# Performance work log

Measured on AMD Instinct MI355X. Metric: run time of the kernel, lower is better.

## Reference

```python
import jax, jax.numpy as jnp
import numpy as np

EPS = 1e-5
QB = 127.0  # int8 activation quantization bound

def rmsnorm(x):
    # SimpleRMSNorm: x / rms(x), no learned scale
    return x * jax.lax.rsqrt(jnp.mean(x * x, axis=-1, keepdims=True) + EPS)

def activation_quant(x):
    # per-token absmax int8 quant-dequant
    scale = QB / jnp.clip(jnp.max(jnp.abs(x), axis=-1, keepdims=True), EPS)
    return jnp.clip(jnp.round(x * scale), -QB - 1, QB) / scale

def weight_quant(w):
    # per-tensor ternary quant-dequant (BitNet b1.58)
    scale = 1.0 / jnp.clip(jnp.mean(jnp.abs(w)), EPS)
    return jnp.clip(jnp.round(w * scale), -1.0, 1.0) / scale

def ste(x, q):
    # straight-through estimator: forward uses q, gradient flows to x
    return x + jax.lax.stop_gradient(q - x)

def bitlinear(x, w, b):
    xn = rmsnorm(x)
    xq = ste(xn, activation_quant(xn))
    wq = ste(w, weight_quant(w))
    # x: [b, s, d_in], w: [d_out, d_in] -> [b, s, d_out]
    return jnp.einsum('bsd,od->bso', xq, wq) + b

def setup_inputs() -> dict:
    key = jax.random.key(0)
    k1, k2, k3, k4, k5 = jax.random.split(key, 5)
    dim, inner = 1024, 4096
    x = jax.random.normal(k1, (4, 4096, dim), dtype=jnp.float32)
    w1 = jax.random.normal(k2, (inner, dim), dtype=jnp.float32) * (dim ** -0.5)
    b1 = jax.random.normal(k3, (inner,), dtype=jnp.float32) * 0.02
    w2 = jax.random.normal(k4, (dim, inner), dtype=jnp.float32) * (inner ** -0.5)
    b2 = jax.random.normal(k5, (dim,), dtype=jnp.float32) * 0.02
    return {"x": x, "w1": w1, "b1": b1, "w2": w2, "b2": b2}

def reference(x, w1, b1, w2, b2):
    h = jax.nn.gelu(bitlinear(x, w1, b1), approximate=False)  # torch nn.GELU default = exact erf
    # dropout p=0.0 is identity; post_act_ln disabled
    return bitlinear(h, w2, b2)
```

## Files before the change

### kernel.cpp

```cpp
#include <hip/hip_runtime.h>
#include <hip/hip_bf16.h>

#define TOK   16384
#define DIM   1024
#define INNER 4096
#define EPSF  1e-5f

typedef int v4i  __attribute__((ext_vector_type(4)));
typedef int v16i __attribute__((ext_vector_type(16)));

static __device__ __forceinline__ void async_copy16(const char* g, char* l) {
    __builtin_amdgcn_global_load_lds(
        (const __attribute__((address_space(1))) unsigned int*)g,
        (__attribute__((address_space(3))) unsigned int*)l, 16, 0, 0);
}

static __device__ __forceinline__ float bf2f(unsigned short u) {
    return __uint_as_float(((unsigned)u) << 16);
}
static __device__ __forceinline__ unsigned short f2bf(float f) {
    unsigned u = __float_as_uint(f);
    return (unsigned short)((u + 0x7fffu + ((u >> 16) & 1u)) >> 16);
}

static __device__ __forceinline__ float fast_erf(float z) {
    float az = fabsf(z);
    float tt = __builtin_amdgcn_rcpf(1.f + 0.3275911f * az);
    float poly = ((((1.061405429f * tt - 1.453152027f) * tt + 1.421413741f) * tt
                   - 0.284496736f) * tt + 0.254829592f) * tt;
    float er = 1.f - poly * __expf(-az * az);
    return copysignf(er, z);
}

static __device__ __forceinline__ float waveSum(float v) {
#pragma unroll
    for (int o = 32; o > 0; o >>= 1) v += __shfl_down(v, o, 64);
    return v;
}
static __device__ __forceinline__ float waveMax(float v) {
#pragma unroll
    for (int o = 32; o > 0; o >>= 1) v = fmaxf(v, __shfl_down(v, o, 64));
    return v;
}

__global__ void absmean_k(const float* __restrict__ w, int n4, float* __restrict__ acc) {
    int idx = blockIdx.x * blockDim.x + threadIdx.x;
    int stride = gridDim.x * blockDim.x;
    const float4* w4 = (const float4*)w;
    float s = 0.f;
    for (int i = idx; i < n4; i += stride) {
        float4 v = w4[i];
        s += fabsf(v.x) + fabsf(v.y) + fabsf(v.z) + fabsf(v.w);
    }
    __shared__ float sp[4];
    int wv = threadIdx.x >> 6, lane = threadIdx.x & 63;
    s = waveSum(s);
    if (lane == 0) sp[wv] = s;
    __syncthreads();
    if (threadIdx.x == 0) atomicAdd(acc, sp[0] + sp[1] + sp[2] + sp[3]);
}

__global__ void wquant_k(const float* __restrict__ w, int n,
                         const float* __restrict__ acc, float* __restrict__ wscale,
                         char* __restrict__ wq) {
    float mean = *acc / (float)n;
    float cl = fmaxf(mean, EPSF);
    float s = 1.f / cl;
    if (blockIdx.x == 0 && threadIdx.x == 0) *wscale = cl;
    int idx = blockIdx.x * blockDim.x + threadIdx.x;
    int stride = gridDim.x * blockDim.x;
    int n4 = n >> 2;
    const float4* w4 = (const float4*)w;
    unsigned* q4 = (unsigned*)wq;
    for (int i = idx; i < n4; i += stride) {
        float4 v = w4[i];
        float e[4] = {v.x, v.y, v.z, v.w};
        unsigned packed = 0;
#pragma unroll
        for (int j = 0; j < 4; j++) {
            float r = rintf(e[j] * s);
            r = fminf(fmaxf(r, -1.f), 1.f);
            packed |= ((unsigned)((int)r & 0xff)) << (8 * j);
        }
        q4[i] = packed;
    }
}

template <int D, int VPT>
__global__ void actquant_f32_k(const float* __restrict__ X, char* __restrict__ Q,
                               float* __restrict__ rs_out) {
    int token = blockIdx.x;
    int t = threadIdx.x;
    const float4* xp = (const float4*)(X + (long)token * D);
    float vals[VPT];
    float ss = 0.f, am = 0.f;
#pragma unroll
    for (int j = 0; j < VPT / 4; j++) {
        float4 v = xp[t * (VPT / 4) + j];
        vals[4 * j] = v.x; vals[4 * j + 1] = v.y; vals[4 * j + 2] = v.z; vals[4 * j + 3] = v.w;
        ss += v.x * v.x + v.y * v.y + v.z * v.z + v.w * v.w;
        am = fmaxf(am, fmaxf(fmaxf(fabsf(v.x), fabsf(v.y)), fmaxf(fabsf(v.z), fabsf(v.w))));
    }
    __shared__ float sp[8];
    __shared__ float bc[2];
    int wv = t >> 6, lane = t & 63;
    float S = waveSum(ss);
    float M = waveMax(am);
    if (lane == 0) { sp[wv] = S; sp[4 + wv] = M; }
    __syncthreads();
    if (t == 0) {
        float Sa = sp[0] + sp[1] + sp[2] + sp[3];
        float Ma = fmaxf(fmaxf(sp[4], sp[5]), fmaxf(sp[6], sp[7]));
        float rinv = rsqrtf(Sa * (1.f / (float)D) + EPSF);
        float amn = Ma * rinv;
        float scale = 127.f / fmaxf(amn, EPSF);
        rs_out[token] = 1.f / scale;
        bc[0] = rinv; bc[1] = scale;
    }
    __syncthreads();
    float rinv = bc[0], scale = bc[1];
    unsigned outw[VPT / 4];
#pragma unroll
    for (int j = 0; j < VPT; j++) {
        float r = rintf((vals[j] * rinv) * scale);
        r = fminf(fmaxf(r, -128.f), 127.f);
        unsigned qi = (unsigned)((int)r & 0xff) << (8 * (j & 3));
        if ((j & 3) == 0) outw[j / 4] = qi; else outw[j / 4] |= qi;
    }
    unsigned* qp = (unsigned*)(Q + (long)token * D);
#pragma unroll
    for (int j = 0; j < VPT / 4; j++) qp[t * (VPT / 4) + j] = outw[j];
}

template <int D, int VPT>
__global__ void actquant_bf16_k(const unsigned short* __restrict__ X, char* __restrict__ Q,
                                float* __restrict__ rs_out) {
    int token = blockIdx.x;
    int t = threadIdx.x;
    const uint4* xp = (const uint4*)(X + (long)token * D);
    float vals[VPT];
    float ss = 0.f, am = 0.f;
#pragma unroll
    for (int j = 0; j < VPT / 8; j++) {
        uint4 v = xp[t * (VPT / 8) + j];
        unsigned ws[4] = {v.x, v.y, v.z, v.w};
#pragma unroll
        for (int p = 0; p < 4; p++) {
            float f0 = bf2f((unsigned short)(ws[p] & 0xffff));
            float f1 = bf2f((unsigned short)(ws[p] >> 16));
            vals[8 * j + 2 * p] = f0; vals[8 * j + 2 * p + 1] = f1;
            ss += f0 * f0 + f1 * f1;
            am = fmaxf(am, fmaxf(fabsf(f0), fabsf(f1)));
        }
    }
    __shared__ float sp[8];
    __shared__ float bc[2];
    int wv = t >> 6, lane = t & 63;
    float S = waveSum(ss);
    float M = waveMax(am);
    if (lane == 0) { sp[wv] = S; sp[4 + wv] = M; }
    __syncthreads();
    if (t == 0) {
        float Sa = sp[0] + sp[1] + sp[2] + sp[3];
        float Ma = fmaxf(fmaxf(sp[4], sp[5]), fmaxf(sp[6], sp[7]));
        float rinv = rsqrtf(Sa * (1.f / (float)D) + EPSF);
        float amn = Ma * rinv;
        float scale = 127.f / fmaxf(amn, EPSF);
        rs_out[token] = 1.f / scale;
        bc[0] = rinv; bc[1] = scale;
    }
    __syncthreads();
    float rinv = bc[0], scale = bc[1];
    unsigned outw[4];
#pragma unroll
    for (int j = 0; j < VPT; j++) {
        float r = rintf((vals[j] * rinv) * scale);
        r = fminf(fmaxf(r, -128.f), 127.f);
        unsigned qi = (unsigned)((int)r & 0xff) << (8 * (j & 3));
        if ((j & 3) == 0) outw[j / 4] = qi; else outw[j / 4] |= qi;
    }
    uint4* qp = (uint4*)(Q + (long)token * D);
    qp[t] = make_uint4(outw[0], outw[1], outw[2], outw[3]);
}

template <int DO_GELU, int OUT_F32>
__global__ __launch_bounds__(256, 2) void gemm_i8_k(
    const char* __restrict__ A, const char* __restrict__ Bw,
    const float* __restrict__ rs, const float* __restrict__ wscale_p,
    const float* __restrict__ bias, void* __restrict__ outp,
    int M, int N, int K) {
    __shared__ char As[2][16384];
    __shared__ char Bs[2][8192];
    int t = threadIdx.x;
    int n0 = blockIdx.x * 128, m0 = blockIdx.y * 256;
    int wv = t >> 6, lane = t & 63;
    int l31 = lane & 31, kh = lane >> 5;
    int wm = (wv & 1) * 128, wn = (wv >> 1) * 64;

    int r = t >> 2;
    const char* aps[4];
    const char* bps[2];
#pragma unroll
    for (int c = 0; c < 4; c++) {
        int row = c * 64 + r;
        int src = (t & 3) ^ ((row >> 1) & 3);
        aps[c] = A + (long)(m0 + row) * K + src * 16;
    }
#pragma unroll
    for (int c = 0; c < 2; c++) {
        int row = c * 64 + r;
        int src = (t & 3) ^ ((row >> 1) & 3);
        bps[c] = Bw + (long)(n0 + row) * K + src * 16;
    }

    v16i acc[4][2] = {};
    int aidx[4][2], bidx[2][2];
#pragma unroll
    for (int i = 0; i < 4; i++) {
        int row = wm + i * 32 + l31;
        int sw = (row >> 1) & 3;
#pragma unroll
        for (int ks = 0; ks < 2; ks++) aidx[i][ks] = row * 4 + ((ks * 2 + kh) ^ sw);
    }
#pragma unroll
    for (int j = 0; j < 2; j++) {
        int row = wn + j * 32 + l31;
        int sw = (row >> 1) & 3;
#pragma unroll
        for (int ks = 0; ks < 2; ks++) bidx[j][ks] = row * 4 + ((ks * 2 + kh) ^ sw);
    }

    auto issue = [&](int it, int buf) {
        long k0 = (long)it << 6;
#pragma unroll
        for (int c = 0; c < 4; c++) async_copy16(aps[c] + k0, As[buf] + c * 4096 + t * 16);
#pragma unroll
        for (int c = 0; c < 2; c++) async_copy16(bps[c] + k0, Bs[buf] + c * 4096 + t * 16);
    };

    int nIt = K >> 6;
    issue(0, 0);
    for (int it = 0; it < nIt; ++it) {
        int cur = it & 1;
        if (it + 1 < nIt) {
            issue(it + 1, cur ^ 1);
            asm volatile("s_waitcnt vmcnt(6)" ::: "memory");
        } else {
            asm volatile("s_waitcnt vmcnt(0)" ::: "memory");
        }
        asm volatile("s_barrier" ::: "memory");
        const v4i* As4 = (const v4i*)As[cur];
        const v4i* Bs4 = (const v4i*)Bs[cur];
#pragma unroll
        for (int ks = 0; ks < 2; ks++) {
            v4i a[4], b[2];
#pragma unroll
            for (int i = 0; i < 4; i++) a[i] = As4[aidx[i][ks]];
#pragma unroll
            for (int j = 0; j < 2; j++) b[j] = Bs4[bidx[j][ks]];
#pragma unroll
            for (int i = 0; i < 4; i++)
#pragma unroll
                for (int j = 0; j < 2; j++)
                    acc[i][j] = __builtin_amdgcn_mfma_i32_32x32x32_i8(a[i], b[j], acc[i][j], 0, 0, 0);
        }
        asm volatile("s_barrier" ::: "memory");
    }

    float wsc = *wscale_p;
    float bv[2];
#pragma unroll
    for (int j = 0; j < 2; j++) bv[j] = bias[n0 + wn + j * 32 + l31];
#pragma unroll
    for (int i = 0; i < 4; i++) {
        int mbase = m0 + wm + i * 32 + 4 * kh;
        float fsv[16];
#pragma unroll
        for (int rg = 0; rg < 16; rg++)
            fsv[rg] = rs[mbase + (rg & 3) + 8 * (rg >> 2)] * wsc;
#pragma unroll
        for (int j = 0; j < 2; j++) {
            int ng = n0 + wn + j * 32 + l31;
#pragma unroll
            for (int rg = 0; rg < 16; rg++) {
                int mg = mbase + (rg & 3) + 8 * (rg >> 2);
                float v = (float)acc[i][j][rg] * fsv[rg] + bv[j];
                if (DO_GELU) v = 0.5f * v * (1.f + fast_erf(v * 0.70710678118654752f));
                long idx = (long)mg * N + ng;
                if (OUT_F32) ((float*)outp)[idx] = v;
                else ((unsigned short*)outp)[idx] = f2bf(v);
            }
        }
    }
}

extern "C" void kernel_launch(void* const* d_in, const int* in_sizes, int n_in,
                              void* d_out, int out_size, void* d_ws, size_t ws_size,
                              hipStream_t stream) {
    const float* x  = (const float*)d_in[0];
    const float* w1 = (const float*)d_in[1];
    const float* b1 = (const float*)d_in[2];
    const float* w2 = (const float*)d_in[3];
    const float* b2 = (const float*)d_in[4];
    float* out = (float*)d_out;

    char* ws = (char*)d_ws;
    float* acc1 = (float*)(ws + 0);
    float* acc2 = (float*)(ws + 4);
    float* wsc1 = (float*)(ws + 8);
    float* wsc2 = (float*)(ws + 12);
    size_t off = 256;
    char* w1q = ws + off; off += (size_t)INNER * DIM;
    char* w2q = ws + off; off += (size_t)INNER * DIM;
    char* xq1 = ws + off; off += (size_t)TOK * DIM;
    float* rs1 = (float*)(ws + off); off += (size_t)TOK * 4;
    char* xq2 = ws + off; off += (size_t)TOK * INNER;
    float* rs2 = (float*)(ws + off); off += (size_t)TOK * 4;
    unsigned short* h = (unsigned short*)(ws + off);

    hipMemsetAsync(d_ws, 0, 16, stream);

    int nw = INNER * DIM;
    absmean_k<<<1024, 256, 0, stream>>>(w1, nw / 4, acc1);
    absmean_k<<<1024, 256, 0, stream>>>(w2, nw / 4, acc2);
    wquant_k<<<2048, 256, 0, stream>>>(w1, nw, acc1, wsc1, w1q);
    wquant_k<<<2048, 256, 0, stream>>>(w2, nw, acc2, wsc2, w2q);

    actquant_f32_k<DIM, 4><<<TOK, 256, 0, stream>>>(x, xq1, rs1);
    gemm_i8_k<1, 0><<<dim3(INNER / 128, TOK / 256), 256, 0, stream>>>(
        xq1, w1q, rs1, wsc1, b1, (void*)h, TOK, INNER, DIM);
    actquant_bf16_k<INNER, 16><<<TOK, 256, 0, stream>>>(h, xq2, rs2);
    gemm_i8_k<0, 1><<<dim3(DIM / 128, TOK / 256), 256, 0, stream>>>(
        xq2, w2q, rs2, wsc2, b2, (void*)out, TOK, DIM, INNER);
}
```

Measured before the change: 421.3 us.

## Restructure int8 GEMM into 256x256 tiles with 8 waves and interleaved prefetch

Replaces the 256x128 int8 MFMA GEMM with a 256x256 tile, 512-thread kernel that uses 128-wide K steps, 128KB LDS double buffering and XOR swizzling. Global-to-LDS loads are staggered between four MFMA phases, separated by barriers and raised wave priority. GELU moves out of the first GEMM epilogue into the bf16 activation-quant kernel. The aim is more data reuse per tile and better overlap of loads with MFMA work, at the cost of heavy LDS use and many barriers that may limit occupancy.

Result: faster. 391.4 us (-7.1%).

```diff
diff --git a/kernel.cpp b/kernel.cpp
--- a/kernel.cpp
+++ b/kernel.cpp
@@ -1,5 +1,4 @@
 #include <hip/hip_runtime.h>
-#include <hip/hip_bf16.h>
 
 #define TOK   16384
 #define DIM   1024
@@ -30,6 +29,9 @@
                    - 0.284496736f) * tt + 0.254829592f) * tt;
     float er = 1.f - poly * __expf(-az * az);
     return copysignf(er, z);
+}
+static __device__ __forceinline__ float gelu_exact(float v) {
+    return 0.5f * v * (1.f + fast_erf(v * 0.70710678118654752f));
 }
 
 static __device__ __forceinline__ float waveSum(float v) {
@@ -146,8 +148,8 @@
         unsigned ws[4] = {v.x, v.y, v.z, v.w};
 #pragma unroll
         for (int p = 0; p < 4; p++) {
-            float f0 = bf2f((unsigned short)(ws[p] & 0xffff));
-            float f1 = bf2f((unsigned short)(ws[p] >> 16));
+            float f0 = gelu_exact(bf2f((unsigned short)(ws[p] & 0xffff)));
+            float f1 = gelu_exact(bf2f((unsigned short)(ws[p] >> 16)));
             vals[8 * j + 2 * p] = f0; vals[8 * j + 2 * p + 1] = f1;
             ss += f0 * f0 + f1 * f1;
             am = fmaxf(am, fmaxf(fabsf(f0), fabsf(f1)));
@@ -183,109 +185,146 @@
     qp[t] = make_uint4(outw[0], outw[1], outw[2], outw[3]);
 }
 
-template <int DO_GELU, int OUT_F32>
-__global__ __launch_bounds__(256, 2) void gemm_i8_k(
+template <int OUT_F32>
+__global__ __launch_bounds__(512, 2) void gemm8_k(
     const char* __restrict__ A, const char* __restrict__ Bw,
     const float* __restrict__ rs, const float* __restrict__ wscale_p,
     const float* __restrict__ bias, void* __restrict__ outp,
     int M, int N, int K) {
-    __shared__ char As[2][16384];
-    __shared__ char Bs[2][8192];
+    __shared__ char L[131072];
     int t = threadIdx.x;
-    int n0 = blockIdx.x * 128, m0 = blockIdx.y * 256;
-    int wv = t >> 6, lane = t & 63;
+    int lane = t & 63, wv = t >> 6;
     int l31 = lane & 31, kh = lane >> 5;
-    int wm = (wv & 1) * 128, wn = (wv >> 1) * 64;
-
-    int r = t >> 2;
-    const char* aps[4];
-    const char* bps[2];
-#pragma unroll
-    for (int c = 0; c < 4; c++) {
-        int row = c * 64 + r;
-        int src = (t & 3) ^ ((row >> 1) & 3);
-        aps[c] = A + (long)(m0 + row) * K + src * 16;
-    }
-#pragma unroll
-    for (int c = 0; c < 2; c++) {
-        int row = c * 64 + r;
-        int src = (t & 3) ^ ((row >> 1) & 3);
-        bps[c] = Bw + (long)(n0 + row) * K + src * 16;
-    }
+    int wmi = wv >> 2, wni = wv & 3;
+    int m0 = blockIdx.y * 256, n0 = blockIdx.x * 256;
+
+    int srow = t >> 3;
+    int scol = ((t & 7) ^ (srow & 7)) * 16;
+    const char* srcA = A + (long)(m0 + srow) * K + scol;
+    const char* srcB = Bw + (long)(n0 + srow) * K + scol;
+    char* ldsA = L + (size_t)t * 16;
+    char* ldsB = L + 65536 + (size_t)t * 16;
+    long k64 = (long)64 * K;
+
+    auto stA = [&](int Tt, int half) {
+        const char* g = srcA + (long)(half * 128) * K + (long)Tt * 128;
+        char* l = ldsA + (Tt & 1) * 32768 + half * 16384;
+        async_copy16(g, l);
+        async_copy16(g + k64, l + 8192);
+    };
+    auto stB = [&](int Tt, int half) {
+        const char* g = srcB + (long)(half * 128) * K + (long)Tt * 128;
+        char* l = ldsB + (Tt & 1) * 32768 + half * 16384;
+        async_copy16(g, l);
+        async_copy16(g + k64, l + 8192);
+    };
+
+    int slot[4];
+#pragma unroll
+    for (int ks = 0; ks < 4; ks++) slot[ks] = ((2 * ks + kh) ^ (l31 & 7)) * 16;
+    int rowA[2][2], rowB[2];
+#pragma unroll
+    for (int ih = 0; ih < 2; ih++)
+#pragma unroll
+        for (int il = 0; il < 2; il++)
+            rowA[ih][il] = (ih * 128 + il * 64 + wmi * 32 + l31) * 128;
+#pragma unroll
+    for (int jh = 0; jh < 2; jh++) rowB[jh] = 65536 + (jh * 128 + wni * 32 + l31) * 128;
 
     v16i acc[4][2] = {};
-    int aidx[4][2], bidx[2][2];
-#pragma unroll
-    for (int i = 0; i < 4; i++) {
-        int row = wm + i * 32 + l31;
-        int sw = (row >> 1) & 3;
-#pragma unroll
-        for (int ks = 0; ks < 2; ks++) aidx[i][ks] = row * 4 + ((ks * 2 + kh) ^ sw);
-    }
-#pragma unroll
-    for (int j = 0; j < 2; j++) {
-        int row = wn + j * 32 + l31;
-        int sw = (row >> 1) & 3;
-#pragma unroll
-        for (int ks = 0; ks < 2; ks++) bidx[j][ks] = row * 4 + ((ks * 2 + kh) ^ sw);
-    }
-
-    auto issue = [&](int it, int buf) {
-        long k0 = (long)it << 6;
-#pragma unroll
-        for (int c = 0; c < 4; c++) async_copy16(aps[c] + k0, As[buf] + c * 4096 + t * 16);
-#pragma unroll
-        for (int c = 0; c < 2; c++) async_copy16(bps[c] + k0, Bs[buf] + c * 4096 + t * 16);
-    };
-
-    int nIt = K >> 6;
-    issue(0, 0);
-    for (int it = 0; it < nIt; ++it) {
-        int cur = it & 1;
-        if (it + 1 < nIt) {
-            issue(it + 1, cur ^ 1);
-            asm volatile("s_waitcnt vmcnt(6)" ::: "memory");
-        } else {
-            asm volatile("s_waitcnt vmcnt(0)" ::: "memory");
-        }
-        asm volatile("s_barrier" ::: "memory");
-        const v4i* As4 = (const v4i*)As[cur];
-        const v4i* Bs4 = (const v4i*)Bs[cur];
-#pragma unroll
-        for (int ks = 0; ks < 2; ks++) {
-            v4i a[4], b[2];
-#pragma unroll
-            for (int i = 0; i < 4; i++) a[i] = As4[aidx[i][ks]];
-#pragma unroll
-            for (int j = 0; j < 2; j++) b[j] = Bs4[bidx[j][ks]];
-#pragma unroll
-            for (int i = 0; i < 4; i++)
-#pragma unroll
-                for (int j = 0; j < 2; j++)
-                    acc[i][j] = __builtin_amdgcn_mfma_i32_32x32x32_i8(a[i], b[j], acc[i][j], 0, 0, 0);
-        }
+    int nK = K >> 7;
+
+    stA(0, 0); stA(0, 1); stB(0, 0); stB(0, 1);
+    stB(1, 0); stA(1, 1);
+    asm volatile("s_waitcnt vmcnt(4)" ::: "memory");
+    asm volatile("s_barrier" ::: "memory");
+
+#pragma unroll 2
+    for (int T = 0; T < nK; ++T) {
+        int bo = (T & 1) * 32768;
+        v4i a[2][4], bb[4];
+#pragma unroll
+        for (int il = 0; il < 2; il++)
+#pragma unroll
+            for (int ks = 0; ks < 4; ks++)
+                a[il][ks] = *(const v4i*)(L + bo + rowA[0][il] + slot[ks]);
+#pragma unroll
+        for (int ks = 0; ks < 4; ks++)
+            bb[ks] = *(const v4i*)(L + bo + rowB[0] + slot[ks]);
+        if (T + 1 < nK) stA(T + 1, 0);
+        asm volatile("s_barrier" ::: "memory");
+        __builtin_amdgcn_s_setprio(1);
+#pragma unroll
+        for (int ks = 0; ks < 4; ks++) {
+            acc[0][0] = __builtin_amdgcn_mfma_i32_32x32x32_i8(a[0][ks], bb[ks], acc[0][0], 0, 0, 0);
+            acc[1][0] = __builtin_amdgcn_mfma_i32_32x32x32_i8(a[1][ks], bb[ks], acc[1][0], 0, 0, 0);
+        }
+        __builtin_amdgcn_s_setprio(0);
+        asm volatile("s_barrier" ::: "memory");
+#pragma unroll
+        for (int il = 0; il < 2; il++)
+#pragma unroll
+            for (int ks = 0; ks < 4; ks++)
+                a[il][ks] = *(const v4i*)(L + bo + rowA[1][il] + slot[ks]);
+        if (T + 1 < nK) stB(T + 1, 1);
+        asm volatile("s_barrier" ::: "memory");
+        __builtin_amdgcn_s_setprio(1);
+#pragma unroll
+        for (int ks = 0; ks < 4; ks++) {
+            acc[2][0] = __builtin_amdgcn_mfma_i32_32x32x32_i8(a[0][ks], bb[ks], acc[2][0], 0, 0, 0);
+            acc[3][0] = __builtin_amdgcn_mfma_i32_32x32x32_i8(a[1][ks], bb[ks], acc[3][0], 0, 0, 0);
+        }
+        __builtin_amdgcn_s_setprio(0);
+        asm volatile("s_barrier" ::: "memory");
+#pragma unroll
+        for (int ks = 0; ks < 4; ks++)
+            bb[ks] = *(const v4i*)(L + bo + rowB[1] + slot[ks]);
+        if (T + 2 < nK) stB(T + 2, 0);
+        asm volatile("s_barrier" ::: "memory");
+        __builtin_amdgcn_s_setprio(1);
+#pragma unroll
+        for (int ks = 0; ks < 4; ks++) {
+            acc[2][1] = __builtin_amdgcn_mfma_i32_32x32x32_i8(a[0][ks], bb[ks], acc[2][1], 0, 0, 0);
+            acc[3][1] = __builtin_amdgcn_mfma_i32_32x32x32_i8(a[1][ks], bb[ks], acc[3][1], 0, 0, 0);
+        }
+        __builtin_amdgcn_s_setprio(0);
+        asm volatile("s_barrier" ::: "memory");
+#pragma unroll
+        for (int il = 0; il < 2; il++)
+#pragma unroll
+            for (int ks = 0; ks < 4; ks++)
+                a[il][ks] = *(const v4i*)(L + bo + rowA[0][il] + slot[ks]);
+        if (T + 2 < nK) stA(T + 2, 1);
+        asm volatile("s_barrier" ::: "memory");
+        __builtin_amdgcn_s_setprio(1);
+#pragma unroll
+        for (int ks = 0; ks < 4; ks++) {
+            acc[0][1] = __builtin_amdgcn_mfma_i32_32x32x32_i8(a[0][ks], bb[ks], acc[0][1], 0, 0, 0);
+            acc[1][1] = __builtin_amdgcn_mfma_i32_32x32x32_i8(a[1][ks], bb[ks], acc[1][1], 0, 0, 0);
+        }
+        __builtin_amdgcn_s_setprio(0);
+        asm volatile("s_waitcnt vmcnt(4)" ::: "memory");
         asm volatile("s_barrier" ::: "memory");
     }
 
     float wsc = *wscale_p;
     float bv[2];
 #pragma unroll
-    for (int j = 0; j < 2; j++) bv[j] = bias[n0 + wn + j * 32 + l31];
+    for (int j = 0; j < 2; j++) bv[j] = bias[n0 + j * 128 + wni * 32 + l31];
 #pragma unroll
     for (int i = 0; i < 4; i++) {
-        int mbase = m0 + wm + i * 32 + 4 * kh;
+        int mbase = m0 + i * 64 + wmi * 32 + 4 * kh;
         float fsv[16];
 #pragma unroll
         for (int rg = 0; rg < 16; rg++)
             fsv[rg] = rs[mbase + (rg & 3) + 8 * (rg >> 2)] * wsc;
 #pragma unroll
         for (int j = 0; j < 2; j++) {
-            int ng = n0 + wn + j * 32 + l31;
+            int ng = n0 + j * 128 + wni * 32 + l31;
 #pragma unroll
             for (int rg = 0; rg < 16; rg++) {
                 int mg = mbase + (rg & 3) + 8 * (rg >> 2);
                 float v = (float)acc[i][j][rg] * fsv[rg] + bv[j];
-                if (DO_GELU) v = 0.5f * v * (1.f + fast_erf(v * 0.70710678118654752f));
                 long idx = (long)mg * N + ng;
                 if (OUT_F32) ((float*)outp)[idx] = v;
                 else ((unsigned short*)outp)[idx] = f2bf(v);
@@ -327,9 +366,9 @@
     wquant_k<<<2048, 256, 0, stream>>>(w2, nw, acc2, wsc2, w2q);
 
     actquant_f32_k<DIM, 4><<<TOK, 256, 0, stream>>>(x, xq1, rs1);
-    gemm_i8_k<1, 0><<<dim3(INNER / 128, TOK / 256), 256, 0, stream>>>(
+    gemm8_k<0><<<dim3(INNER / 256, TOK / 256), 512, 0, stream>>>(
         xq1, w1q, rs1, wsc1, b1, (void*)h, TOK, INNER, DIM);
     actquant_bf16_k<INNER, 16><<<TOK, 256, 0, stream>>>(h, xq2, rs2);
-    gemm_i8_k<0, 1><<<dim3(DIM / 128, TOK / 256), 256, 0, stream>>>(
+    gemm8_k<1><<<dim3(DIM / 256, TOK / 256), 512, 0, stream>>>(
         xq2, w2q, rs2, wsc2, b2, (void*)out, TOK, DIM, INNER);
 }
```
